# Kernel optimization log

Measured on AMD Instinct MI355X. Metric: run time of the kernel, lower is better.

The kernel has to match this reference:

```python
import jax, jax.numpy as jnp
import numpy as np
import math

H_DIM = 512
QKV_DIM = 512
NUM_HEADS = 8
HEAD_DIM = QKV_DIM // NUM_HEADS
B, S = 4, 8192


def setup_inputs() -> dict:
    key = jax.random.key(0)
    ks = jax.random.split(key, 9)
    sc = 1.0 / math.sqrt(H_DIM)
    return {
        "x": jax.random.normal(ks[0], (B, S, H_DIM), dtype=jnp.float32),
        "Wq": jax.random.normal(ks[1], (QKV_DIM, H_DIM), dtype=jnp.float32) * sc,
        "bq": jax.random.normal(ks[2], (QKV_DIM,), dtype=jnp.float32) * 0.01,
        "Wk": jax.random.normal(ks[3], (QKV_DIM, H_DIM), dtype=jnp.float32) * sc,
        "bk": jax.random.normal(ks[4], (QKV_DIM,), dtype=jnp.float32) * 0.01,
        "Wv": jax.random.normal(ks[5], (QKV_DIM, H_DIM), dtype=jnp.float32) * sc,
        "bv": jax.random.normal(ks[6], (QKV_DIM,), dtype=jnp.float32) * 0.01,
        "Wl": jax.random.normal(ks[7], (H_DIM, QKV_DIM), dtype=jnp.float32) * sc,
        "bl": jax.random.normal(ks[8], (H_DIM,), dtype=jnp.float32) * 0.01,
    }


def _split_heads(t):
    # [B, S, QKV] -> [B, num_heads, S, head_dim]
    Bn, Sn, _ = t.shape
    return t.reshape(Bn, Sn, NUM_HEADS, HEAD_DIM).transpose(0, 2, 1, 3)


def reference(x, Wq, bq, Wk, bk, Wv, bv, Wl, bl):
    # self-attention: k = v = q = x
    q = _split_heads(x @ Wq.T + bq)
    k = _split_heads(x @ Wk.T + bk)
    v = _split_heads(x @ Wv.T + bv)
    seq_len = q.shape[2]
    # kv: [B, H, head_dim, head_dim] -- tiny intermediate, scaled by 1/sqrt(S)
    kv = jnp.einsum('bhsd,bhse->bhde', k, v) * (1.0 / math.sqrt(seq_len))
    # dropout_rate = 0.0 -> identity
    out = jnp.einsum('bhsd,bhde->bhse', q, kv)  # [B, H, S, head_dim]
    out = out.transpose(0, 2, 1, 3).reshape(x.shape[0], seq_len, QKV_DIM)
    return out @ Wl.T + bl
```

## Files before the change

### kernel.cpp

```cpp
#include <hip/hip_runtime.h>
#include <hip/hip_bf16.h>

#define DEVI __device__ __forceinline__

typedef __bf16 bf16x8 __attribute__((ext_vector_type(8)));
typedef __bf16 bf16x4 __attribute__((ext_vector_type(4)));
typedef float  f32x4  __attribute__((ext_vector_type(4)));

constexpr int Bn = 4, Sn = 8192, Hn = 512;
constexpr float INV_SQRT_S = 0.011048543456039806f;

#define GLOAD16(gp, lp) __builtin_amdgcn_global_load_lds(                      \
    (const __attribute__((address_space(1))) unsigned int*)(gp),               \
    (__attribute__((address_space(3))) unsigned int*)(lp), 16, 0, 0)

DEVI void split2(float v, __bf16* h, __bf16* l) {
  __bf16 hh = (__bf16)v; *h = hh; *l = (__bf16)(v - (float)hh);
}

__global__ __launch_bounds__(256) void k0_split(const float* __restrict__ x,
    __bf16* __restrict__ xh, __bf16* __restrict__ xl,
    __bf16* __restrict__ xhT, __bf16* __restrict__ xlT, float* __restrict__ ssum)
{
  __shared__ __bf16 lh[64*68], ll[64*68];
  __shared__ float csum[64];
  int wg = blockIdx.x;
  int ct = wg & 7, st = (wg >> 3) & 127, b = wg >> 10;
  int s0 = st * 64, c0 = ct * 64;
  int t = threadIdx.x, r0 = t >> 4, c4 = t & 15;
  if (t < 64) csum[t] = 0.f;
  __syncthreads();
  float sloc[4] = {0.f, 0.f, 0.f, 0.f};
#pragma unroll
  for (int i = 0; i < 4; ++i) {
    int r = r0 + 16 * i;
    size_t base = ((size_t)(b * Sn + s0 + r)) * Hn + c0 + c4 * 4;
    float4 v = *(const float4*)(x + base);
    __bf16 h[4], l[4];
    split2(v.x, &h[0], &l[0]); split2(v.y, &h[1], &l[1]);
    split2(v.z, &h[2], &l[2]); split2(v.w, &h[3], &l[3]);
    *(bf16x4*)(xh + base) = (bf16x4){h[0], h[1], h[2], h[3]};
    *(bf16x4*)(xl + base) = (bf16x4){l[0], l[1], l[2], l[3]};
#pragma unroll
    for (int j = 0; j < 4; ++j) {
      lh[(c4 * 4 + j) * 68 + r] = h[j];
      ll[(c4 * 4 + j) * 68 + r] = l[j];
    }
    sloc[0] += v.x; sloc[1] += v.y; sloc[2] += v.z; sloc[3] += v.w;
  }
#pragma unroll
  for (int j = 0; j < 4; ++j) atomicAdd(&csum[c4 * 4 + j], sloc[j]);
  __syncthreads();
#pragma unroll
  for (int i = 0; i < 4; ++i) {
    int cr = r0 + 16 * i;
    size_t tb = ((size_t)(b * Hn + c0 + cr)) * Sn + s0 + c4 * 4;
    *(bf16x4*)(xhT + tb) = *(const bf16x4*)(lh + cr * 68 + c4 * 4);
    *(bf16x4*)(xlT + tb) = *(const bf16x4*)(ll + cr * 68 + c4 * 4);
  }
  if (t < 64) atomicAdd(&ssum[b * Hn + c0 + t], csum[t]);
}

__global__ __launch_bounds__(256) void k0w_weights(
    const float* __restrict__ Wq, const float* __restrict__ Wk,
    const float* __restrict__ Wv, const float* __restrict__ Wl,
    __bf16* WqTh, __bf16* WqTl, __bf16* Wkh, __bf16* Wkl,
    __bf16* Wvh, __bf16* Wvl, __bf16* Wlh, __bf16* Wll)
{
  __shared__ __bf16 lh[64*68], ll[64*68];
  int wg = blockIdx.x;
  int ct = wg & 7, st = (wg >> 3) & 7, arr = wg >> 6;
  int t = threadIdx.x, r0 = t >> 4, c4 = t & 15;
  int rbase = st * 64, cbase = ct * 64;
  const float* src = (arr == 0) ? Wk : (arr == 1) ? Wv : (arr == 2) ? Wl : Wq;
  __bf16* dh = (arr == 0) ? Wkh : (arr == 1) ? Wvh : Wlh;
  __bf16* dl = (arr == 0) ? Wkl : (arr == 1) ? Wvl : Wll;
#pragma unroll
  for (int i = 0; i < 4; ++i) {
    int r = r0 + 16 * i;
    size_t base = ((size_t)(rbase + r)) * 512 + cbase + c4 * 4;
    float4 v = *(const float4*)(src + base);
    __bf16 h[4], l[4];
    split2(v.x, &h[0], &l[0]); split2(v.y, &h[1], &l[1]);
    split2(v.z, &h[2], &l[2]); split2(v.w, &h[3], &l[3]);
    if (arr < 3) {
      *(bf16x4*)(dh + base) = (bf16x4){h[0], h[1], h[2], h[3]};
      *(bf16x4*)(dl + base) = (bf16x4){l[0], l[1], l[2], l[3]};
    } else {
#pragma unroll
      for (int j = 0; j < 4; ++j) {
        lh[(c4 * 4 + j) * 68 + r] = h[j];
        ll[(c4 * 4 + j) * 68 + r] = l[j];
      }
    }
  }
  if (arr == 3) {
    __syncthreads();
#pragma unroll
    for (int i = 0; i < 4; ++i) {
      int cr = r0 + 16 * i;
      size_t tb = ((size_t)(cbase + cr)) * 512 + rbase + c4 * 4;
      *(bf16x4*)(WqTh + tb) = *(const bf16x4*)(lh + cr * 68 + c4 * 4);
      *(bf16x4*)(WqTl + tb) = *(const bf16x4*)(ll + cr * 68 + c4 * 4);
    }
  }
}

DEVI void stage128(const __bf16* src, int ld, __bf16* dst, int wave, int lane) {
#pragma unroll
  for (int i = 0; i < 4; ++i) {
    int g = i * 256 + wave * 64 + lane;
    int row = g >> 3, kk = (g & 7) * 8;
    GLOAD16(src + (size_t)row * ld + kk, dst + (size_t)(i * 256 + wave * 64) * 8);
  }
}

DEVI void frag_compute128(const __bf16* As, const __bf16* Bs, int lane, int wr, int wc,
                          f32x4 acc[4][4]) {
#pragma unroll
  for (int kk = 0; kk < 64; kk += 32) {
    bf16x8 a[4], bb[4];
#pragma unroll
    for (int mf = 0; mf < 4; ++mf)
      a[mf] = *(const bf16x8*)(As + (size_t)(wr * 64 + mf * 16 + (lane & 15)) * 64 + kk + (lane >> 4) * 8);
#pragma unroll
    for (int nf = 0; nf < 4; ++nf)
      bb[nf] = *(const bf16x8*)(Bs + (size_t)(wc * 64 + nf * 16 + (lane & 15)) * 64 + kk + (lane >> 4) * 8);
#pragma unroll
    for (int mf = 0; mf < 4; ++mf)
#pragma unroll
      for (int nf = 0; nf < 4; ++nf)
        acc[mf][nf] = __builtin_amdgcn_mfma_f32_16x16x32_bf16(a[mf], bb[nf], acc[mf][nf], 0, 0, 0);
  }
}

__global__ __launch_bounds__(256) void k1_pr(const __bf16* __restrict__ xhT,
                                             const __bf16* __restrict__ xlT,
                                             float* __restrict__ PR)
{
  __shared__ alignas(16) __bf16 lds[2][2][128 * 64];
  int bid = blockIdx.x;
  int wgid = (bid & 7) * 64 + (bid >> 3);
  int nt = wgid & 7, mt = (wgid >> 3) & 3, kc = (wgid >> 5) & 3, b = wgid >> 7;
  int t = threadIdx.x, wave = t >> 6, lane = t & 63, wr = wave >> 1, wc = wave & 1;
  const __bf16* A = xhT + ((size_t)(b * Hn + mt * 128)) * Sn;
  const __bf16* Bp = (nt < 4) ? xhT + ((size_t)(b * Hn + nt * 128)) * Sn
                              : xlT + ((size_t)(b * Hn + (nt - 4) * 128)) * Sn;
  int k0 = kc * 2048;
  f32x4 acc[4][4];
#pragma unroll
  for (int mf = 0; mf < 4; ++mf)
#pragma unroll
    for (int nf = 0; nf < 4; ++nf)
#pragma unroll
      for (int r = 0; r < 4; ++r) acc[mf][nf][r] = 0.f;

  stage128(A + k0, Sn, lds[0][0], wave, lane);
  stage128(Bp + k0, Sn, lds[0][1], wave, lane);
  __syncthreads();
  for (int st = 0; st < 32; ++st) {
    int cur = st & 1;
    if (st < 31) {
      stage128(A + k0 + (st + 1) * 64, Sn, lds[1 - cur][0], wave, lane);
      stage128(Bp + k0 + (st + 1) * 64, Sn, lds[1 - cur][1], wave, lane);
    }
    frag_compute128(lds[cur][0], lds[cur][1], lane, wr, wc, acc);
    __syncthreads();
  }
#pragma unroll
  for (int mf = 0; mf < 4; ++mf)
#pragma unroll
    for (int nf = 0; nf < 4; ++nf) {
      int m = mt * 128 + wr * 64 + mf * 16 + (lane >> 4) * 4;
      int n = nt * 128 + wc * 64 + nf * 16 + (lane & 15);
      float* dst = PR + (((size_t)kc * 4 + b) * 512 + m) * 1024 + n;
#pragma unroll
      for (int r = 0; r < 4; ++r) dst[(size_t)r * 1024] = acc[mf][nf][r];
    }
}

__global__ __launch_bounds__(256) void k2a_gasm(const float* __restrict__ PR,
                                                __bf16* __restrict__ Gh, __bf16* __restrict__ Gl)
{
  __shared__ float tr[64 * 68];
  constexpr size_t SLAB = (size_t)4 * 512 * 1024;
  int wg = blockIdx.x;
  int qt = wg & 7, pt = (wg >> 3) & 7, b = wg >> 6;
  int p0 = pt * 64, q0 = qt * 64;
  int t = threadIdx.x, r0 = t >> 4, c4 = t & 15;
#pragma unroll
  for (int i = 0; i < 4; ++i) {
    int rr = r0 + 16 * i, cc = c4 * 4;
    size_t off = ((size_t)(b * 512) + q0 + rr) * 1024 + 512 + p0 + cc;
    float4 v = {0.f, 0.f, 0.f, 0.f};
#pragma unroll
    for (int kc = 0; kc < 4; ++kc) {
      float4 u = *(const float4*)(PR + kc * SLAB + off);
      v.x += u.x; v.y += u.y; v.z += u.z; v.w += u.w;
    }
    tr[(cc + 0) * 68 + rr] = v.x; tr[(cc + 1) * 68 + rr] = v.y;
    tr[(cc + 2) * 68 + rr] = v.z; tr[(cc + 3) * 68 + rr] = v.w;
  }
  __syncthreads();
#pragma unroll
  for (int i = 0; i < 4; ++i) {
    int r = r0 + 16 * i, c = c4 * 4;
    size_t rb = ((size_t)(b * 512) + p0 + r) * 1024;
    float4 P4 = {0.f, 0.f, 0.f, 0.f}, R4 = {0.f, 0.f, 0.f, 0.f};
#pragma unroll
    for (int kc = 0; kc < 4; ++kc) {
      float4 u = *(const float4*)(PR + kc * SLAB + rb + q0 + c);
      float4 w = *(const float4*)(PR + kc * SLAB + rb + 512 + q0 + c);
      P4.x += u.x; P4.y += u.y; P4.z += u.z; P4.w += u.w;
      R4.x += w.x; R4.y += w.y; R4.z += w.z; R4.w += w.w;
    }
    float g[4] = {P4.x + R4.x + tr[r * 68 + c + 0], P4.y + R4.y + tr[r * 68 + c + 1],
                  P4.z + R4.z + tr[r * 68 + c + 2], P4.w + R4.w + tr[r * 68 + c + 3]};
    __bf16 h[4], l[4];
#pragma unroll
    for (int j = 0; j < 4; ++j) split2(g[j], &h[j], &l[j]);
    size_t o = ((size_t)(b * 512) + p0 + r) * 512 + q0 + c;
    *(bf16x4*)(Gh + o) = (bf16x4){h[0], h[1], h[2], h[3]};
    *(bf16x4*)(Gl + o) = (bf16x4){l[0], l[1], l[2], l[3]};
  }
}

DEVI void stage64(const __bf16* src, int ld, __bf16* dst, int wave, int lane) {
#pragma unroll
  for (int i = 0; i < 2; ++i) {
    int g = i * 256 + wave * 64 + lane;
    int row = g >> 3, kk = (g & 7) * 8;
    GLOAD16(src + (size_t)row * ld + kk, dst + (size_t)(i * 256 + wave * 64) * 8);
  }
}

DEVI void gemm3_64(const __bf16* Ah, const __bf16* Al, int lda,
                   const __bf16* Bh, const __bf16* Bl, int ldb,
                   int K, __bf16* lds, int t, f32x4 acc[2][2])
{
  int wave = t >> 6, lane = t & 63, wr = wave >> 1, wc = wave & 1;
#pragma unroll
  for (int mf = 0; mf < 2; ++mf)
#pragma unroll
    for (int nf = 0; nf < 2; ++nf)
#pragma unroll
      for (int r = 0; r < 4; ++r) acc[mf][nf][r] = 0.f;
  for (int ks = 0; ks < K; ks += 64) {
    stage64(Ah + ks, lda, lds + 0 * 4096, wave, lane);
    stage64(Al + ks, lda, lds + 1 * 4096, wave, lane);
    stage64(Bh + ks, ldb, lds + 2 * 4096, wave, lane);
    stage64(Bl + ks, ldb, lds + 3 * 4096, wave, lane);
    __syncthreads();
#pragma unroll
    for (int kk = 0; kk < 64; kk += 32) {
      bf16x8 ah[2], al[2], bh[2], bl[2];
#pragma unroll
      for (int mf = 0; mf < 2; ++mf) {
        int ro = (wr * 32 + mf * 16 + (lane & 15)) * 64 + kk + (lane >> 4) * 8;
        ah[mf] = *(const bf16x8*)(lds + 0 * 4096 + ro);
        al[mf] = *(const bf16x8*)(lds + 1 * 4096 + ro);
      }
#pragma unroll
      for (int nf = 0; nf < 2; ++nf) {
        int ro = (wc * 32 + nf * 16 + (lane & 15)) * 64 + kk + (lane >> 4) * 8;
        bh[nf] = *(const bf16x8*)(lds + 2 * 4096 + ro);
        bl[nf] = *(const bf16x8*)(lds + 3 * 4096 + ro);
      }
#pragma unroll
      for (int mf = 0; mf < 2; ++mf)
#pragma unroll
        for (int nf = 0; nf < 2; ++nf) {
          acc[mf][nf] = __builtin_amdgcn_mfma_f32_16x16x32_bf16(ah[mf], bh[nf], acc[mf][nf], 0, 0, 0);
          acc[mf][nf] = __builtin_amdgcn_mfma_f32_16x16x32_bf16(ah[mf], bl[nf], acc[mf][nf], 0, 0, 0);
          acc[mf][nf] = __builtin_amdgcn_mfma_f32_16x16x32_bf16(al[mf], bh[nf], acc[mf][nf], 0, 0, 0);
        }
    }
    __syncthreads();
  }
}

__global__ __launch_bounds__(256) void kA_gw(const __bf16* Gh, const __bf16* Gl,
                                             const __bf16* Wvh, const __bf16* Wvl,
                                             __bf16* GWTh, __bf16* GWTl)
{
  __shared__ alignas(16) __bf16 lds[4 * 4096];
  __shared__ float trf[64 * 68];
  int wg = blockIdx.x;
  int pt = wg & 7, h = (wg >> 3) & 7, b = wg >> 6;
  int t = threadIdx.x;
  f32x4 acc[2][2];
  gemm3_64(Gh + ((size_t)(b * 512 + pt * 64)) * 512,
           Gl + ((size_t)(b * 512 + pt * 64)) * 512, 512,
           Wvh + (size_t)(h * 64) * 512, Wvl + (size_t)(h * 64) * 512, 512,
           512, lds, t, acc);
  int wave = t >> 6, lane = t & 63, wr = wave >> 1, wc = wave & 1;
#pragma unroll
  for (int mf = 0; mf < 2; ++mf)
#pragma unroll
    for (int nf = 0; nf < 2; ++nf)
#pragma unroll
      for (int r = 0; r < 4; ++r) {
        int m = wr * 32 + mf * 16 + (lane >> 4) * 4 + r;
        int n = wc * 32 + nf * 16 + (lane & 15);
        trf[m * 68 + n] = acc[mf][nf][r];
      }
  __syncthreads();
  int e_ = t >> 2, pseg = (t & 3) * 16;
  size_t rowbase = (((size_t)b * 8 + h) * 64 + e_) * 512 + pt * 64 + pseg;
#pragma unroll
  for (int seg = 0; seg < 2; ++seg) {
    bf16x8 vh, vl;
#pragma unroll
    for (int j = 0; j < 8; ++j) {
      __bf16 hh, ll; split2(trf[(pseg + seg * 8 + j) * 68 + e_], &hh, &ll);
      vh[j] = hh; vl[j] = ll;
    }
    *(bf16x8*)(GWTh + rowbase + seg * 8) = vh;
    *(bf16x8*)(GWTl + rowbase + seg * 8) = vl;
  }
}

__global__ __launch_bounds__(256) void kB_kv(const __bf16* Wkh, const __bf16* Wkl,
    const __bf16* GWTh, const __bf16* GWTl,
    const float* __restrict__ Wk, const float* __restrict__ Wv,
    const float* __restrict__ ssum, const float* __restrict__ bq,
    const float* __restrict__ bk, const float* __restrict__ bv,
    __bf16* kvTh, __bf16* kvTl, float* bqkv)
{
  __shared__ alignas(16) __bf16 lds[4 * 4096];
  __shared__ float kvl[64 * 65];
  __shared__ float wks[64], wvs[64], red[256];
  int wg = blockIdx.x;
  int h = wg & 7, b = wg >> 3;
  int t = threadIdx.x;
  f32x4 acc[2][2];
  gemm3_64(Wkh + (size_t)(h * 64) * 512, Wkl + (size_t)(h * 64) * 512, 512,
           GWTh + ((size_t)b * 8 + h) * 64 * 512,
           GWTl + ((size_t)b * 8 + h) * 64 * 512, 512,
           512, lds, t, acc);
  int wave = t >> 6, lane = t & 63, wr = wave >> 1, wc = wave & 1;
#pragma unroll
  for (int mf = 0; mf < 2; ++mf)
#pragma unroll
    for (int nf = 0; nf < 2; ++nf)
#pragma unroll
      for (int r = 0; r < 4; ++r) {
        int m = wr * 32 + mf * 16 + (lane >> 4) * 4 + r;
        int n = wc * 32 + nf * 16 + (lane & 15);
        kvl[m * 65 + n] = acc[mf][nf][r];
      }
  int row = t & 63, part = t >> 6;
  const float* sb = ssum + b * 512 + part * 128;
  {
    const float4* wr4 = (const float4*)(Wk + (size_t)(h * 64 + row) * 512 + part * 128);
    float p1 = 0.f;
#pragma unroll
    for (int i = 0; i < 32; ++i) {
      float4 w = wr4[i];
      p1 += w.x * sb[i * 4] + w.y * sb[i * 4 + 1] + w.z * sb[i * 4 + 2] + w.w * sb[i * 4 + 3];
    }
    red[t] = p1;
  }
  __syncthreads();
  if (t < 64) wks[t] = red[t] + red[t + 64] + red[t + 128] + red[t + 192];
  __syncthreads();
  {
    const float4* wr4 = (const float4*)(Wv + (size_t)(h * 64 + row) * 512 + part * 128);
    float p1 = 0.f;
#pragma unroll
    for (int i = 0; i < 32; ++i) {
      float4 w = wr4[i];
      p1 += w.x * sb[i * 4] + w.y * sb[i * 4 + 1] + w.z * sb[i * 4 + 2] + w.w * sb[i * 4 + 3];
    }
    red[t] = p1;
  }
  __syncthreads();
  if (t < 64) wvs[t] = red[t] + red[t + 64] + red[t + 128] + red[t + 192];
  __syncthreads();
  {
    int d = t >> 2, eseg = (t & 3) * 16;
    float bkd = bk[h * 64 + d], wksd = wks[d];
#pragma unroll
    for (int j = 0; j < 16; ++j) {
      int e = eseg + j;
      float bve = bv[h * 64 + e];
      float v = kvl[d * 65 + e] + wksd * bve + bkd * wvs[e] + 8192.0f * bkd * bve;
      kvl[d * 65 + e] = v * INV_SQRT_S;
    }
  }
  __syncthreads();
  if (t < 64) {
    int e = t;
    float a2 = 0.f;
    for (int dd = 0; dd < 64; ++dd) a2 += bq[h * 64 + dd] * kvl[dd * 65 + e];
    bqkv[b * 512 + h * 64 + e] = a2;
  }
  {
    int e = t >> 2, dseg = (t & 3) * 16;
    size_t rowbase = (((size_t)b * 8 + h) * 64 + e) * 64 + dseg;
#pragma unroll
    for (int seg = 0; seg < 2; ++seg) {
      bf16x8 vh, vl;
#pragma unroll
      for (int j = 0; j < 8; ++j) {
        __bf16 hh, ll; split2(kvl[(dseg + seg * 8 + j) * 65 + e], &hh, &ll);
        vh[j] = hh; vl[j] = ll;
      }
      *(bf16x8*)(kvTh + rowbase + seg * 8) = vh;
      *(bf16x8*)(kvTl + rowbase + seg * 8) = vl;
    }
  }
}

__global__ __launch_bounds__(256) void k2u(const __bf16* WqTh, const __bf16* WqTl,
                                           const __bf16* kvTh, const __bf16* kvTl,
                                           __bf16* Uh, __bf16* Ul)
{
  __shared__ alignas(16) __bf16 lds[4 * 4096];
  int wg = blockIdx.x;
  int ib = wg & 7, h = (wg >> 3) & 7, b = wg >> 6;
  int t = threadIdx.x;
  f32x4 acc[2][2];
  gemm3_64(WqTh + (size_t)(ib * 64) * 512 + h * 64,
           WqTl + (size_t)(ib * 64) * 512 + h * 64, 512,
           kvTh + ((size_t)b * 8 + h) * 4096,
           kvTl + ((size_t)b * 8 + h) * 4096, 64, 64, lds, t, acc);
  int wave = t >> 6, lane = t & 63, wr = wave >> 1, wc = wave & 1;
#pragma unroll
  for (int mf = 0; mf < 2; ++mf)
#pragma unroll
    for (int nf = 0; nf < 2; ++nf)
#pragma unroll
      for (int r = 0; r < 4; ++r) {
        int m = ib * 64 + wr * 32 + mf * 16 + (lane >> 4) * 4 + r;
        int n = h * 64 + wc * 32 + nf * 16 + (lane & 15);
        __bf16 hh, ll; split2(acc[mf][nf][r], &hh, &ll);
        size_t o = ((size_t)(b * 512) + m) * 512 + n;
        Uh[o] = hh; Ul[o] = ll;
      }
}

__global__ __launch_bounds__(256) void k2weff(const __bf16* Uh, const __bf16* Ul,
                                              const __bf16* Wlh, const __bf16* Wll,
                                              __bf16* WTh, __bf16* WTl)
{
  __shared__ alignas(16) __bf16 lds[4 * 4096];
  __shared__ float trf[64 * 68];
  int wg = blockIdx.x;
  int jb = wg & 7, ib = (wg >> 3) & 7, b = wg >> 6;
  int t = threadIdx.x;
  f32x4 acc[2][2];
  gemm3_64(Uh + ((size_t)(b * 512 + ib * 64)) * 512,
           Ul + ((size_t)(b * 512 + ib * 64)) * 512, 512,
           Wlh + (size_t)(jb * 64) * 512, Wll + (size_t)(jb * 64) * 512, 512,
           512, lds, t, acc);
  int wave = t >> 6, lane = t & 63, wr = wave >> 1, wc = wave & 1;
#pragma unroll
  for (int mf = 0; mf < 2; ++mf)
#pragma unroll
    for (int nf = 0; nf < 2; ++nf)
#pragma unroll
      for (int r = 0; r < 4; ++r) {
        int m = wr * 32 + mf * 16 + (lane >> 4) * 4 + r;
        int n = wc * 32 + nf * 16 + (lane & 15);
        trf[m * 68 + n] = acc[mf][nf][r];
      }
  __syncthreads();
  int n_ = t >> 2, mseg = (t & 3) * 16;
  size_t rowbase = ((size_t)(b * 512 + jb * 64 + n_)) * 512 + ib * 64 + mseg;
#pragma unroll
  for (int seg = 0; seg < 2; ++seg) {
    bf16x8 vh, vl;
#pragma unroll
    for (int j = 0; j < 8; ++j) {
      __bf16 hh, ll; split2(trf[(mseg + seg * 8 + j) * 68 + n_], &hh, &ll);
      vh[j] = hh; vl[j] = ll;
    }
    *(bf16x8*)(WTh + rowbase + seg * 8) = vh;
    *(bf16x8*)(WTl + rowbase + seg * 8) = vl;
  }
}

__global__ __launch_bounds__(512) void k2beff(const float* bqkv, const float* Wl,
                                              const float* bl, float* beff)
{
  __shared__ float bq_s[512];
  int b = blockIdx.x, j = threadIdx.x;
  bq_s[j] = bqkv[b * 512 + j];
  __syncthreads();
  const float4* wrow = (const float4*)(Wl + (size_t)j * 512);
  float acc = bl[j];
  for (int m4 = 0; m4 < 128; ++m4) {
    float4 w = wrow[m4];
    acc += w.x * bq_s[m4 * 4] + w.y * bq_s[m4 * 4 + 1] + w.z * bq_s[m4 * 4 + 2] + w.w * bq_s[m4 * 4 + 3];
  }
  beff[b * 512 + j] = acc;
}

__global__ __launch_bounds__(256) void k3_final(const __bf16* __restrict__ xh,
    const __bf16* __restrict__ xl, const __bf16* __restrict__ WTh,
    const __bf16* __restrict__ WTl, const float* __restrict__ beff,
    float* __restrict__ out)
{
  __shared__ alignas(16) __bf16 lds[2][2][128 * 64];
  int bid = blockIdx.x;
  int wgid = (bid & 7) * 128 + (bid >> 3);
  int nt = wgid & 3, mt = (wgid >> 2) & 63, b = wgid >> 8;
  int t = threadIdx.x, wave = t >> 6, lane = t & 63, wr = wave >> 1, wc = wave & 1;
  const __bf16* Axh = xh + ((size_t)(b * Sn + mt * 128)) * Hn;
  const __bf16* Axl = xl + ((size_t)(b * Sn + mt * 128)) * Hn;
  const __bf16* Bh = WTh + ((size_t)(b * Hn + nt * 128)) * Hn;
  const __bf16* Bl = WTl + ((size_t)(b * Hn + nt * 128)) * Hn;
  f32x4 acc[4][4];
#pragma unroll
  for (int mf = 0; mf < 4; ++mf)
#pragma unroll
    for (int nf = 0; nf < 4; ++nf)
#pragma unroll
      for (int r = 0; r < 4; ++r) acc[mf][nf][r] = 0.f;

  stage128(Axh, Hn, lds[0][0], wave, lane);
  stage128(Bh, Hn, lds[0][1], wave, lane);
  __syncthreads();
  for (int st = 0; st < 24; ++st) {
    int cur = st & 1;
    if (st < 23) {
      int nst = st + 1, term = nst >> 3, kcol = (nst & 7) * 64;
      const __bf16* As = (term == 2) ? Axl : Axh;
      const __bf16* Bs = (term == 1) ? Bl : Bh;
      stage128(As + kcol, Hn, lds[1 - cur][0], wave, lane);
      stage128(Bs + kcol, Hn, lds[1 - cur][1], wave, lane);
    }
    frag_compute128(lds[cur][0], lds[cur][1], lane, wr, wc, acc);
    __syncthreads();
  }
#pragma unroll
  for (int mf = 0; mf < 4; ++mf)
#pragma unroll
    for (int nf = 0; nf < 4; ++nf) {
      int n = nt * 128 + wc * 64 + nf * 16 + (lane & 15);
      float be = beff[b * Hn + n];
      int m0 = mt * 128 + wr * 64 + mf * 16 + (lane >> 4) * 4;
#pragma unroll
      for (int r = 0; r < 4; ++r)
        out[((size_t)(b * Sn) + m0 + r) * Hn + n] = acc[mf][nf][r] + be;
    }
}

extern "C" void kernel_launch(void* const* d_in, const int* in_sizes, int n_in,
                              void* d_out, int out_size, void* d_ws, size_t ws_size,
                              hipStream_t stream)
{
  (void)in_sizes; (void)n_in; (void)out_size; (void)ws_size;
  const float* x  = (const float*)d_in[0];
  const float* Wq = (const float*)d_in[1];
  const float* bq = (const float*)d_in[2];
  const float* Wk = (const float*)d_in[3];
  const float* bk = (const float*)d_in[4];
  const float* Wv = (const float*)d_in[5];
  const float* bv = (const float*)d_in[6];
  const float* Wl = (const float*)d_in[7];
  const float* bl = (const float*)d_in[8];
  float* out = (float*)d_out;

  char* p = (char*)d_ws;
  auto alloc = [&](size_t bytes) { char* r = p; p += (bytes + 255) & ~(size_t)255; return r; };
  const size_t XB = (size_t)Bn * Sn * Hn * 2;
  __bf16* xh  = (__bf16*)alloc(XB);
  __bf16* xl  = (__bf16*)alloc(XB);
  __bf16* xhT = (__bf16*)alloc(XB);
  __bf16* xlT = (__bf16*)alloc(XB);
  float*  PR  = (float*)alloc((size_t)4 * Bn * 512 * 1024 * 4);
  float*  ssum = (float*)alloc((size_t)Bn * 512 * 4);
  const size_t WB = 512 * 512 * 2;
  __bf16* WqTh = (__bf16*)alloc(WB); __bf16* WqTl = (__bf16*)alloc(WB);
  __bf16* Wkh  = (__bf16*)alloc(WB); __bf16* Wkl  = (__bf16*)alloc(WB);
  __bf16* Wvh  = (__bf16*)alloc(WB); __bf16* Wvl  = (__bf16*)alloc(WB);
  __bf16* Wlh  = (__bf16*)alloc(WB); __bf16* Wll  = (__bf16*)alloc(WB);
  float*  bqkv = (float*)alloc((size_t)Bn * 512 * 4);
  float*  beff = (float*)alloc((size_t)Bn * 512 * 4);

  char* q = (char*)xhT;
  auto alloc2 = [&](size_t bytes) { char* r = q; q += (bytes + 255) & ~(size_t)255; return r; };
  __bf16* Gh   = (__bf16*)alloc2((size_t)Bn * 512 * 512 * 2);
  __bf16* Gl   = (__bf16*)alloc2((size_t)Bn * 512 * 512 * 2);
  __bf16* GWTh = (__bf16*)alloc2((size_t)Bn * 8 * 64 * 512 * 2);
  __bf16* GWTl = (__bf16*)alloc2((size_t)Bn * 8 * 64 * 512 * 2);
  __bf16* kvTh = (__bf16*)alloc2((size_t)Bn * 8 * 64 * 64 * 2);
  __bf16* kvTl = (__bf16*)alloc2((size_t)Bn * 8 * 64 * 64 * 2);
  __bf16* Uh   = (__bf16*)alloc2((size_t)Bn * 512 * 512 * 2);
  __bf16* Ul   = (__bf16*)alloc2((size_t)Bn * 512 * 512 * 2);
  __bf16* WTh  = (__bf16*)alloc2((size_t)Bn * 512 * 512 * 2);
  __bf16* WTl  = (__bf16*)alloc2((size_t)Bn * 512 * 512 * 2);

  hipMemsetAsync(ssum, 0, (size_t)Bn * 512 * 4, stream);

  k0_split<<<4096, 256, 0, stream>>>(x, xh, xl, xhT, xlT, ssum);
  k0w_weights<<<256, 256, 0, stream>>>(Wq, Wk, Wv, Wl, WqTh, WqTl, Wkh, Wkl, Wvh, Wvl, Wlh, Wll);
  k1_pr<<<512, 256, 0, stream>>>(xhT, xlT, PR);
  k2a_gasm<<<256, 256, 0, stream>>>(PR, Gh, Gl);
  kA_gw<<<256, 256, 0, stream>>>(Gh, Gl, Wvh, Wvl, GWTh, GWTl);
  kB_kv<<<32, 256, 0, stream>>>(Wkh, Wkl, GWTh, GWTl, Wk, Wv, ssum, bq, bk, bv, kvTh, kvTl, bqkv);
  k2u<<<256, 256, 0, stream>>>(WqTh, WqTl, kvTh, kvTl, Uh, Ul);
  k2weff<<<256, 256, 0, stream>>>(Uh, Ul, Wlh, Wll, WTh, WTl);
  k2beff<<<4, 512, 0, stream>>>(bqkv, Wl, bl, beff);
  k3_final<<<1024, 256, 0, stream>>>(xh, xl, WTh, WTl, beff, out);
}
```

Measured before the change: 360.1 us.

## Rework k1 and k3 GEMMs into 8-wave 256x128 tiles with triple-buffered swizzled LDS

The two large GEMM kernels (Gram-matrix k1_pr and final projection k3_final) now use 512-thread workgroups computing 256x128 tiles. They stage through a three-slot LDS ring with XOR-swizzled rows to avoid bank conflicts, and prefetch two k-steps ahead with explicit vmcnt/lgkmcnt waits. Each k-step is split into two halves so global loads interleave with MFMA bursts, and s_setprio raises priority around the MFMA blocks. This targets exposed memory latency and LDS bank conflicts, at the cost of 144KB LDS per block and fragile hand-placed wait counts.

Measured after the change: 338.7 us. 6.0% less time.

```diff
diff --git a/kernel.cpp b/kernel.cpp
--- a/kernel.cpp
+++ b/kernel.cpp
@@ -13,6 +13,12 @@
 #define GLOAD16(gp, lp) __builtin_amdgcn_global_load_lds(                      \
     (const __attribute__((address_space(1))) unsigned int*)(gp),               \
     (__attribute__((address_space(3))) unsigned int*)(lp), 16, 0, 0)
+
+#define SCHED0 __builtin_amdgcn_sched_barrier(0)
+#define SBAR do { SCHED0; __builtin_amdgcn_s_barrier(); SCHED0; } while (0)
+#define WAITV6 do { asm volatile("s_waitcnt vmcnt(6)" ::: "memory"); SCHED0; } while (0)
+#define WAITV0 do { asm volatile("s_waitcnt vmcnt(0)" ::: "memory"); SCHED0; } while (0)
+#define WAITL0 do { asm volatile("s_waitcnt lgkmcnt(0)" ::: "memory"); SCHED0; } while (0)
 
 DEVI void split2(float v, __bf16* h, __bf16* l) {
   __bf16 hh = (__bf16)v; *h = hh; *l = (__bf16)(v - (float)hh);
@@ -106,73 +112,109 @@
   }
 }
 
-DEVI void stage128(const __bf16* src, int ld, __bf16* dst, int wave, int lane) {
-#pragma unroll
-  for (int i = 0; i < 4; ++i) {
-    int g = i * 256 + wave * 64 + lane;
-    int row = g >> 3, kk = (g & 7) * 8;
-    GLOAD16(src + (size_t)row * ld + kk, dst + (size_t)(i * 256 + wave * 64) * 8);
-  }
-}
-
-DEVI void frag_compute128(const __bf16* As, const __bf16* Bs, int lane, int wr, int wc,
-                          f32x4 acc[4][4]) {
-#pragma unroll
-  for (int kk = 0; kk < 64; kk += 32) {
-    bf16x8 a[4], bb[4];
+constexpr int SLOT_BYTES = 49152;
+
+DEVI void stageP(const __bf16* __restrict__ rowbase, int ld, char* region,
+                 int call, int tid) {
+  int D = (call << 13) + (tid << 4);
+  int row = D >> 7;
+  int colb = (D & 127) ^ ((row & 7) << 4);
+  GLOAD16(rowbase + (size_t)row * ld + (colb >> 1),
+          region + (call << 13) + ((tid >> 6) << 10));
+}
+
+DEVI bf16x8 ldsRead(const char* region, int row, int kbyte) {
+  int addr = (row << 7) + (kbyte ^ ((row & 7) << 4));
+  return *(const bf16x8*)(region + addr);
+}
+
+__global__ __launch_bounds__(512, 2) void k1_pr(const __bf16* __restrict__ xhT,
+                                                const __bf16* __restrict__ xlT,
+                                                float* __restrict__ PR)
+{
+  __shared__ alignas(1024) char lds[3 * SLOT_BYTES];
+  int bid = blockIdx.x;
+  int wgid = (bid & 7) * 32 + (bid >> 3);
+  int nt = wgid & 7, mt = (wgid >> 3) & 1, kc = (wgid >> 4) & 3, b = wgid >> 6;
+  int tid = threadIdx.x, lane = tid & 63, w = tid >> 6, wm = w >> 1, wn = w & 1;
+  const __bf16* A = xhT + ((size_t)(b * Hn) + mt * 256) * Sn + kc * 2048;
+  const __bf16* Bp = ((nt < 4) ? xhT + ((size_t)(b * Hn) + nt * 128) * Sn
+                               : xlT + ((size_t)(b * Hn) + (nt - 4) * 128) * Sn) + kc * 2048;
+  f32x4 acc[4][4];
+#pragma unroll
+  for (int mf = 0; mf < 4; ++mf)
+#pragma unroll
+    for (int nf = 0; nf < 4; ++nf)
+#pragma unroll
+      for (int r = 0; r < 4; ++r) acc[mf][nf][r] = 0.f;
+
+  auto stage_half = [&](int kt, int half) {
+    const __bf16* As = A + kt * 64;
+    const __bf16* Bs = Bp + kt * 64;
+    char* aR = lds + (kt % 3) * SLOT_BYTES;
+    char* bR = aR + 32768;
+    if (half == 0) {
+      stageP(As, Sn, aR, 0, tid); stageP(As, Sn, aR, 1, tid); stageP(As, Sn, aR, 2, tid);
+    } else {
+      stageP(As, Sn, aR, 3, tid); stageP(Bs, Sn, bR, 0, tid); stageP(Bs, Sn, bR, 1, tid);
+    }
+  };
+
+  stage_half(0, 0); stage_half(0, 1); stage_half(1, 0); stage_half(1, 1);
+
+  int arow = lane & 15, koff = (lane >> 4) << 4;
+
+  for (int kt = 0; kt < 32; ++kt) {
+    if (kt < 31) { WAITV6; } else { WAITV0; }
+    SBAR;
+    const char* aR = lds + (kt % 3) * SLOT_BYTES;
+    const char* bR = aR + 32768;
+    bf16x8 af[4][2], bfr[2][2];
 #pragma unroll
     for (int mf = 0; mf < 4; ++mf)
-      a[mf] = *(const bf16x8*)(As + (size_t)(wr * 64 + mf * 16 + (lane & 15)) * 64 + kk + (lane >> 4) * 8);
-#pragma unroll
-    for (int nf = 0; nf < 4; ++nf)
-      bb[nf] = *(const bf16x8*)(Bs + (size_t)(wc * 64 + nf * 16 + (lane & 15)) * 64 + kk + (lane >> 4) * 8);
+#pragma unroll
+      for (int kh = 0; kh < 2; ++kh)
+        af[mf][kh] = ldsRead(aR, wm * 64 + mf * 16 + arow, kh * 64 + koff);
+#pragma unroll
+    for (int nf = 0; nf < 2; ++nf)
+#pragma unroll
+      for (int kh = 0; kh < 2; ++kh)
+        bfr[nf][kh] = ldsRead(bR, wn * 64 + nf * 16 + arow, kh * 64 + koff);
+    if (kt < 30) stage_half(kt + 2, 0);
+    WAITL0;
+    __builtin_amdgcn_s_setprio(1);
 #pragma unroll
     for (int mf = 0; mf < 4; ++mf)
 #pragma unroll
-      for (int nf = 0; nf < 4; ++nf)
-        acc[mf][nf] = __builtin_amdgcn_mfma_f32_16x16x32_bf16(a[mf], bb[nf], acc[mf][nf], 0, 0, 0);
-  }
-}
-
-__global__ __launch_bounds__(256) void k1_pr(const __bf16* __restrict__ xhT,
-                                             const __bf16* __restrict__ xlT,
-                                             float* __restrict__ PR)
-{
-  __shared__ alignas(16) __bf16 lds[2][2][128 * 64];
-  int bid = blockIdx.x;
-  int wgid = (bid & 7) * 64 + (bid >> 3);
-  int nt = wgid & 7, mt = (wgid >> 3) & 3, kc = (wgid >> 5) & 3, b = wgid >> 7;
-  int t = threadIdx.x, wave = t >> 6, lane = t & 63, wr = wave >> 1, wc = wave & 1;
-  const __bf16* A = xhT + ((size_t)(b * Hn + mt * 128)) * Sn;
-  const __bf16* Bp = (nt < 4) ? xhT + ((size_t)(b * Hn + nt * 128)) * Sn
-                              : xlT + ((size_t)(b * Hn + (nt - 4) * 128)) * Sn;
-  int k0 = kc * 2048;
-  f32x4 acc[4][4];
+      for (int nf = 0; nf < 2; ++nf)
+#pragma unroll
+        for (int kh = 0; kh < 2; ++kh)
+          acc[mf][nf] = __builtin_amdgcn_mfma_f32_16x16x32_bf16(af[mf][kh], bfr[nf][kh], acc[mf][nf], 0, 0, 0);
+    __builtin_amdgcn_s_setprio(0);
+    SBAR;
+#pragma unroll
+    for (int nf = 0; nf < 2; ++nf)
+#pragma unroll
+      for (int kh = 0; kh < 2; ++kh)
+        bfr[nf][kh] = ldsRead(bR, wn * 64 + (nf + 2) * 16 + arow, kh * 64 + koff);
+    if (kt < 30) stage_half(kt + 2, 1);
+    WAITL0;
+    __builtin_amdgcn_s_setprio(1);
+#pragma unroll
+    for (int mf = 0; mf < 4; ++mf)
+#pragma unroll
+      for (int nf = 0; nf < 2; ++nf)
+#pragma unroll
+        for (int kh = 0; kh < 2; ++kh)
+          acc[mf][nf + 2] = __builtin_amdgcn_mfma_f32_16x16x32_bf16(af[mf][kh], bfr[nf][kh], acc[mf][nf + 2], 0, 0, 0);
+    __builtin_amdgcn_s_setprio(0);
+  }
 #pragma unroll
   for (int mf = 0; mf < 4; ++mf)
 #pragma unroll
-    for (int nf = 0; nf < 4; ++nf)
-#pragma unroll
-      for (int r = 0; r < 4; ++r) acc[mf][nf][r] = 0.f;
-
-  stage128(A + k0, Sn, lds[0][0], wave, lane);
-  stage128(Bp + k0, Sn, lds[0][1], wave, lane);
-  __syncthreads();
-  for (int st = 0; st < 32; ++st) {
-    int cur = st & 1;
-    if (st < 31) {
-      stage128(A + k0 + (st + 1) * 64, Sn, lds[1 - cur][0], wave, lane);
-      stage128(Bp + k0 + (st + 1) * 64, Sn, lds[1 - cur][1], wave, lane);
-    }
-    frag_compute128(lds[cur][0], lds[cur][1], lane, wr, wc, acc);
-    __syncthreads();
-  }
-#pragma unroll
-  for (int mf = 0; mf < 4; ++mf)
-#pragma unroll
     for (int nf = 0; nf < 4; ++nf) {
-      int m = mt * 128 + wr * 64 + mf * 16 + (lane >> 4) * 4;
-      int n = nt * 128 + wc * 64 + nf * 16 + (lane & 15);
+      int m = mt * 256 + wm * 64 + mf * 16 + (lane >> 4) * 4;
+      int n = nt * 128 + wn * 64 + nf * 16 + (lane & 15);
       float* dst = PR + (((size_t)kc * 4 + b) * 512 + m) * 1024 + n;
 #pragma unroll
       for (int r = 0; r < 4; ++r) dst[(size_t)r * 1024] = acc[mf][nf][r];
@@ -497,20 +539,21 @@
   beff[b * 512 + j] = acc;
 }
 
-__global__ __launch_bounds__(256) void k3_final(const __bf16* __restrict__ xh,
+__global__ __launch_bounds__(512, 2) void k3_final(const __bf16* __restrict__ xh,
     const __bf16* __restrict__ xl, const __bf16* __restrict__ WTh,
     const __bf16* __restrict__ WTl, const float* __restrict__ beff,
     float* __restrict__ out)
 {
-  __shared__ alignas(16) __bf16 lds[2][2][128 * 64];
+  __shared__ alignas(1024) char lds[3 * SLOT_BYTES];
   int bid = blockIdx.x;
-  int wgid = (bid & 7) * 128 + (bid >> 3);
-  int nt = wgid & 3, mt = (wgid >> 2) & 63, b = wgid >> 8;
-  int t = threadIdx.x, wave = t >> 6, lane = t & 63, wr = wave >> 1, wc = wave & 1;
-  const __bf16* Axh = xh + ((size_t)(b * Sn + mt * 128)) * Hn;
-  const __bf16* Axl = xl + ((size_t)(b * Sn + mt * 128)) * Hn;
-  const __bf16* Bh = WTh + ((size_t)(b * Hn + nt * 128)) * Hn;
-  const __bf16* Bl = WTl + ((size_t)(b * Hn + nt * 128)) * Hn;
+  int wgid = (bid & 7) * 64 + (bid >> 3);
+  int nt = wgid & 3, mtt = wgid >> 2;
+  int b = mtt >> 5, srow = (mtt & 31) << 8;
+  int tid = threadIdx.x, lane = tid & 63, w = tid >> 6, wm = w >> 1, wn = w & 1;
+  const __bf16* Axh = xh + ((size_t)b * Sn + srow) * Hn;
+  const __bf16* Axl = xl + ((size_t)b * Sn + srow) * Hn;
+  const __bf16* Bh = WTh + ((size_t)b * Hn + nt * 128) * Hn;
+  const __bf16* Bl = WTl + ((size_t)b * Hn + nt * 128) * Hn;
   f32x4 acc[4][4];
 #pragma unroll
   for (int mf = 0; mf < 4; ++mf)
@@ -519,31 +562,78 @@
 #pragma unroll
       for (int r = 0; r < 4; ++r) acc[mf][nf][r] = 0.f;
 
-  stage128(Axh, Hn, lds[0][0], wave, lane);
-  stage128(Bh, Hn, lds[0][1], wave, lane);
-  __syncthreads();
-  for (int st = 0; st < 24; ++st) {
-    int cur = st & 1;
-    if (st < 23) {
-      int nst = st + 1, term = nst >> 3, kcol = (nst & 7) * 64;
-      const __bf16* As = (term == 2) ? Axl : Axh;
-      const __bf16* Bs = (term == 1) ? Bl : Bh;
-      stage128(As + kcol, Hn, lds[1 - cur][0], wave, lane);
-      stage128(Bs + kcol, Hn, lds[1 - cur][1], wave, lane);
-    }
-    frag_compute128(lds[cur][0], lds[cur][1], lane, wr, wc, acc);
-    __syncthreads();
+  auto stage_half = [&](int kt, int half) {
+    int term = kt >> 3, kcol = (kt & 7) << 6;
+    const __bf16* As = ((term == 2) ? Axl : Axh) + kcol;
+    const __bf16* Bs = ((term == 1) ? Bl : Bh) + kcol;
+    char* aR = lds + (kt % 3) * SLOT_BYTES;
+    char* bR = aR + 32768;
+    if (half == 0) {
+      stageP(As, Hn, aR, 0, tid); stageP(As, Hn, aR, 1, tid); stageP(As, Hn, aR, 2, tid);
+    } else {
+      stageP(As, Hn, aR, 3, tid); stageP(Bs, Hn, bR, 0, tid); stageP(Bs, Hn, bR, 1, tid);
+    }
+  };
+
+  stage_half(0, 0); stage_half(0, 1); stage_half(1, 0); stage_half(1, 1);
+
+  int arow = lane & 15, koff = (lane >> 4) << 4;
+
+  for (int kt = 0; kt < 24; ++kt) {
+    if (kt < 23) { WAITV6; } else { WAITV0; }
+    SBAR;
+    const char* aR = lds + (kt % 3) * SLOT_BYTES;
+    const char* bR = aR + 32768;
+    bf16x8 af[4][2], bfr[2][2];
+#pragma unroll
+    for (int mf = 0; mf < 4; ++mf)
+#pragma unroll
+      for (int kh = 0; kh < 2; ++kh)
+        af[mf][kh] = ldsRead(aR, wm * 64 + mf * 16 + arow, kh * 64 + koff);
+#pragma unroll
+    for (int nf = 0; nf < 2; ++nf)
+#pragma unroll
+      for (int kh = 0; kh < 2; ++kh)
+        bfr[nf][kh] = ldsRead(bR, wn * 64 + nf * 16 + arow, kh * 64 + koff);
+    if (kt < 22) stage_half(kt + 2, 0);
+    WAITL0;
+    __builtin_amdgcn_s_setprio(1);
+#pragma unroll
+    for (int mf = 0; mf < 4; ++mf)
+#pragma unroll
+      for (int nf = 0; nf < 2; ++nf)
+#pragma unroll
+        for (int kh = 0; kh < 2; ++kh)
+          acc[mf][nf] = __builtin_amdgcn_mfma_f32_16x16x32_bf16(af[mf][kh], bfr[nf][kh], acc[mf][nf], 0, 0, 0);
+    __builtin_amdgcn_s_setprio(0);
+    SBAR;
+#pragma unroll
+    for (int nf = 0; nf < 2; ++nf)
+#pragma unroll
+      for (int kh = 0; kh < 2; ++kh)
+        bfr[nf][kh] = ldsRead(bR, wn * 64 + (nf + 2) * 16 + arow, kh * 64 + koff);
+    if (kt < 22) stage_half(kt + 2, 1);
+    WAITL0;
+    __builtin_amdgcn_s_setprio(1);
+#pragma unroll
+    for (int mf = 0; mf < 4; ++mf)
+#pragma unroll
+      for (int nf = 0; nf < 2; ++nf)
+#pragma unroll
+        for (int kh = 0; kh < 2; ++kh)
+          acc[mf][nf + 2] = __builtin_amdgcn_mfma_f32_16x16x32_bf16(af[mf][kh], bfr[nf][kh], acc[mf][nf + 2], 0, 0, 0);
+    __builtin_amdgcn_s_setprio(0);
   }
 #pragma unroll
   for (int mf = 0; mf < 4; ++mf)
 #pragma unroll
     for (int nf = 0; nf < 4; ++nf) {
-      int n = nt * 128 + wc * 64 + nf * 16 + (lane & 15);
+      int n = nt * 128 + wn * 64 + nf * 16 + (lane & 15);
       float be = beff[b * Hn + n];
-      int m0 = mt * 128 + wr * 64 + mf * 16 + (lane >> 4) * 4;
+      int m0 = srow + wm * 64 + mf * 16 + (lane >> 4) * 4;
 #pragma unroll
       for (int r = 0; r < 4; ++r)
-        out[((size_t)(b * Sn) + m0 + r) * Hn + n] = acc[mf][nf][r] + be;
+        out[((size_t)b * Sn + m0 + r) * Hn + n] = acc[mf][nf][r] + be;
     }
 }
 
@@ -597,12 +687,12 @@
 
   k0_split<<<4096, 256, 0, stream>>>(x, xh, xl, xhT, xlT, ssum);
   k0w_weights<<<256, 256, 0, stream>>>(Wq, Wk, Wv, Wl, WqTh, WqTl, Wkh, Wkl, Wvh, Wvl, Wlh, Wll);
-  k1_pr<<<512, 256, 0, stream>>>(xhT, xlT, PR);
+  k1_pr<<<256, 512, 0, stream>>>(xhT, xlT, PR);
   k2a_gasm<<<256, 256, 0, stream>>>(PR, Gh, Gl);
   kA_gw<<<256, 256, 0, stream>>>(Gh, Gl, Wvh, Wvl, GWTh, GWTl);
   kB_kv<<<32, 256, 0, stream>>>(Wkh, Wkl, GWTh, GWTl, Wk, Wv, ssum, bq, bk, bv, kvTh, kvTl, bqkv);
   k2u<<<256, 256, 0, stream>>>(WqTh, WqTl, kvTh, kvTl, Uh, Ul);
   k2weff<<<256, 256, 0, stream>>>(Uh, Ul, Wlh, Wll, WTh, WTl);
   k2beff<<<4, 512, 0, stream>>>(bqkv, Wl, bl, beff);
-  k3_final<<<1024, 256, 0, stream>>>(xh, xl, WTh, WTl, beff, out);
-}
+  k3_final<<<512, 512, 0, stream>>>(xh, xl, WTh, WTl, beff, out);
+}
```
